# Kernel optimization log

Measured on AMD Instinct MI355X. Metric: run time of the kernel, lower is better.

The kernel has to match this reference:

```python
import jax, jax.numpy as jnp
import numpy as np

K = 3          # kernel_size (forced by hardcoded padding=1 in query unfold)
PAD = 1        # padding
C_IN = 64      # conv in_channels (x has C_IN + 5 channels)
C_OUT = 128    # out_channels
B, H, W = 16, 32, 32


def unfold(x, k, pad=0, mode='constant'):
    """torch.nn.functional.unfold equivalent. x: (B,C,H,W) -> (B, C*k*k, L).
    Ordering matches torch: channel slowest, then kernel row, then kernel col."""
    if pad:
        x = jnp.pad(x, ((0, 0), (0, 0), (pad, pad), (pad, pad)), mode=mode)
    b, c, h, w = x.shape
    oh, ow = h - k + 1, w - k + 1
    # (B, C, k*k, oh, ow) with patch index i*k+j
    patches = jnp.stack([x[:, :, i:i + oh, j:j + ow]
                         for i in range(k) for j in range(k)], axis=2)
    return patches.reshape(b, c * k * k, oh * ow)


def conv2d(x, w, b, pad):
    out = jax.lax.conv_general_dilated(
        x, w, window_strides=(1, 1), padding=[(pad, pad), (pad, pad)],
        dimension_numbers=('NCHW', 'OIHW', 'NCHW'))
    return out + b[None, :, None, None]


def setup_inputs() -> dict:
    key = jax.random.key(0)
    ks = jax.random.split(key, 6)
    fan1 = C_IN * K * K
    fan2 = C_OUT * 1 * 1
    return {
        'x': jax.random.normal(ks[0], (B, C_IN + 5, H, W), jnp.float32),
        'conv_w': jax.random.normal(ks[1], (C_OUT, C_IN, K, K), jnp.float32) / np.sqrt(fan1),
        'conv_b': jax.random.normal(ks[2], (C_OUT,), jnp.float32) * 0.01,
        'conv2_w': jax.random.normal(ks[3], (1, C_OUT, 1, 1), jnp.float32) / np.sqrt(fan2),
        'conv2_b': jax.random.normal(ks[4], (1,), jnp.float32) * 0.01,
        'shapes_kernel': jax.random.uniform(ks[5], (1, C_OUT, K * K * 5, 1), jnp.float32),
    }


def reference(x, conv_w, conv_b, conv2_w, conv2_b, shapes_kernel):
    k, pad = K, PAD
    center = k * k // 2

    conv_out = conv2d(x[:, :-5], conv_w, conv_b, pad)          # (B, C_OUT, H', W')
    b, cout, oh, ow = conv_out.shape
    L = oh * ow

    # shape-channel windows (replication-padded), center-relative positions
    sw = unfold(x[:, -5:], k, pad, 'edge').reshape(b, 5, k * k, L)
    sw = sw.at[:, 0:2].add(-sw[:, 0:2, center:center + 1])

    # L1 distance of each window to each learned shape kernel
    sd = jnp.abs(sw.reshape(b, 1, 5 * k * k, L) - shapes_kernel).sum(axis=2)  # (B, C_OUT, L)
    sd = sd.reshape(b, cout, oh, ow)

    saf = jax.nn.relu(conv_out / (sd + 1.0))                    # shape_attended_features

    q = conv2d(saf, conv2_w, conv2_b, 0) / jnp.sqrt(jnp.float32(cout))  # (B, 1, H', W')
    qu = jax.nn.softmax(unfold(q, k, 1), axis=1)[:, None]       # (B, 1, k*k, L), zero-padded

    u_mean = unfold(x[:, -5:-3], k, pad, 'edge').reshape(b, 2, k * k, L)
    means = (u_mean * qu).sum(axis=2)                           # (B, 2, L)

    v1 = (unfold(x[:, -3:-1], k, pad, 'edge').reshape(b, 2, k * k, L) * qu).sum(axis=2)
    v2 = (((u_mean - means[:, :, None, :]) ** 2) * qu).sum(axis=2)
    var = v1 + v2                                               # (B, 2, L)

    c1 = (unfold(x[:, -1:], k, pad, 'edge').reshape(b, 1, k * k, L) * qu).sum(axis=2)
    c2 = ((u_mean[:, 0:1] - means[:, 0:1, None, :]) *
          (u_mean[:, 1:2] - means[:, 1:2, None, :]) * qu).sum(axis=2)
    covar = c1 + c2                                             # (B, 1, L)

    agg = jnp.concatenate([means, var, covar], axis=1).reshape(b, 5, oh, ow)
    return jnp.concatenate([saf, agg], axis=1)                  # (B, C_OUT+5, H', W')
```

## Files before the change

kernel.cpp:

```cpp
#include <hip/hip_runtime.h>
#include <math.h>

#define CI 64
#define CO 128
#define CX 69
#define LPIX 1024

typedef __attribute__((ext_vector_type(8))) short bf16x8;
typedef __attribute__((ext_vector_type(4))) float f32x4;

#define WMF_OFF  0
#define SKT_OFF  147456
#define QP_OFF   (147456 + 23040)

__device__ __forceinline__ unsigned short f2bf(float f) {
  unsigned u = __float_as_uint(f);
  unsigned r = (u + 0x7fffu + ((u >> 16) & 1u)) >> 16;
  return (unsigned short)r;
}

__launch_bounds__(256)
__global__ void prepW(const float* __restrict__ cwg,
                      const float* __restrict__ skg,
                      unsigned short* __restrict__ wmf,
                      float* __restrict__ skt) {
  int i = blockIdx.x * 256 + threadIdx.x;
  if (i < 128 * 9 * 64) {
    int co = i / 576, rem = i - co * 576;
    int tap = rem >> 6, ci = rem & 63;
    wmf[i] = f2bf(cwg[co * 576 + ci * 9 + tap]);
  } else {
    int d = i - 128 * 9 * 64;
    if (d < 45 * 128) {
      int j = d >> 7, co = d & 127;
      skt[j * 128 + co] = skg[co * 45 + j];
    }
  }
}

__launch_bounds__(512, 4)
__global__ void convFused(const float* __restrict__ xg,
                          const unsigned short* __restrict__ wmfg,
                          const float* __restrict__ cbg,
                          const float* __restrict__ w2g,
                          const float* __restrict__ sktg,
                          float* __restrict__ qp,
                          float* __restrict__ outg) {
  __shared__ char arena[18432];
  __shared__ float lds_sx[5 * 144];
  __shared__ float qred[8][64];

  unsigned short* ldsB = (unsigned short*)arena;
  float* lds_c = (float*)arena;

  const int tid = threadIdx.x;
  const int blk = blockIdx.x;
  const int coh = blk & 1;
  const int rp  = (blk >> 1) & 15;
  const int b   = blk >> 5;
  const int r0  = rp * 2;

  const int w    = tid >> 6;
  const int lane = tid & 63;
  const int rsel = w >> 2;
  const int ct   = w & 3;
  const int n16  = lane & 15;
  const int kq   = lane >> 4;

  const float* xb = xg + (size_t)b * CX * LPIX;
  const float* xs = xb + CI * LPIX;

  bf16x8 areg[2][9];
  {
    const unsigned short* abase =
        wmfg + (size_t)(coh * 64 + ct * 16 + n16) * 576 + kq * 8;
    #pragma unroll
    for (int ch = 0; ch < 2; ++ch)
      #pragma unroll
      for (int tap = 0; tap < 9; ++tap)
        areg[ch][tap] = *(const bf16x8*)(abase + tap * 64 + ch * 32);
  }

  {
    const int row  = tid >> 7;
    const int cip  = (tid >> 2) & 31;
    const int colq = tid & 3;
    const int ci   = cip * 2;
    const int c0   = colq * 8;
    const int grow = r0 - 1 + row;
    f32x4 u0a = {}, u0b = {}, u1a = {}, u1b = {};
    if ((unsigned)grow < 32u) {
      const float* p0 = xb + ci * LPIX + grow * 32 + c0;
      u0a = *(const f32x4*)p0;          u0b = *(const f32x4*)(p0 + 4);
      u1a = *(const f32x4*)(p0 + LPIX); u1b = *(const f32x4*)(p0 + LPIX + 4);
    }
    #pragma unroll
    for (int cc = 0; cc < 8; ++cc) {
      float f0 = (cc < 4) ? u0a[cc] : u0b[cc - 4];
      float f1 = (cc < 4) ? u1a[cc] : u1b[cc - 4];
      unsigned v = (unsigned)f2bf(f0) | ((unsigned)f2bf(f1) << 16);
      const int slot  = c0 + cc + 1;
      const int gslot = ((ci >> 3) << 3) ^ ((slot & 7) << 3);
      ((unsigned*)ldsB)[(((row * 36 + slot) << 6) + gslot + (ci & 7)) >> 1] = v;
    }
    {
      const int prw = tid >> 7;
      const int s4  = (tid >> 5) & 3;
      const int sl  = (s4 == 0) ? 0 : (32 + s4);
      const int ci2 = (tid & 31) * 2;
      const int gsl = ((ci2 >> 3) << 3) ^ ((sl & 7) << 3);
      ((unsigned*)ldsB)[(((prw * 36 + sl) << 6) + gsl + (ci2 & 7)) >> 1] = 0;
    }
  }

  for (int idx = tid; idx < 5 * 144; idx += 512) {
    int c = idx / 144, rem = idx - c * 144;
    int s = rem / 36, j = rem - s * 36;
    int hh = r0 - 1 + s; hh = hh < 0 ? 0 : (hh > 31 ? 31 : hh);
    int col = j - 1;     col = col < 0 ? 0 : (col > 31 ? 31 : col);
    lds_sx[idx] = xs[c * LPIX + hh * 32 + col];
  }
  __syncthreads();

  f32x4 acc[2] = {};
  #pragma unroll
  for (int tap = 0; tap < 9; ++tap) {
    const int dr = tap / 3, dc = tap % 3;
    const int rowst = rsel + dr;
    #pragma unroll
    for (int ch = 0; ch < 2; ++ch) {
      const int g = (ch << 2) + kq;
      #pragma unroll
      for (int pt = 0; pt < 2; ++pt) {
        const int slot = pt * 16 + n16 + dc;
        const int gs = (g ^ (slot & 7)) << 3;
        bf16x8 bfr = *(const bf16x8*)(ldsB + ((rowst * 36 + slot) << 6) + gs);
        acc[pt] = __builtin_amdgcn_mfma_f32_16x16x32_bf16(areg[ch][tap], bfr,
                                                          acc[pt], 0, 0, 0);
      }
    }
  }
  __syncthreads();

  #pragma unroll
  for (int pt = 0; pt < 2; ++pt) {
    const int pxl = rsel * 32 + pt * 16 + n16;
    const int cog = ct * 4 + kq;
    const int sg  = cog ^ (pxl & 7);
    *(f32x4*)&lds_c[pxl * 64 + sg * 4] = acc[pt];
  }
  __syncthreads();

  const int wS   = __builtin_amdgcn_readfirstlane(w);
  const int co0g = coh * 64 + wS * 8;
  const int pxl  = lane;

  float cvals[8];
  #pragma unroll
  for (int g = 0; g < 2; ++g) {
    const int cog = wS * 2 + g;
    const int sg  = cog ^ (pxl & 7);
    *(f32x4*)&cvals[g * 4] = *(const f32x4*)&lds_c[pxl * 64 + sg * 4];
  }

  const int xbase = (pxl >> 5) * 36 + (pxl & 31);
  float swv[45];
  {
    const float c0 = lds_sx[0 * 144 + 37 + xbase];
    const float c1 = lds_sx[1 * 144 + 37 + xbase];
    #pragma unroll
    for (int c = 0; c < 5; ++c) {
      float ctr = (c == 0) ? c0 : ((c == 1) ? c1 : 0.f);
      #pragma unroll
      for (int s = 0; s < 3; ++s)
        #pragma unroll
        for (int dc = 0; dc < 3; ++dc)
          swv[c * 9 + s * 3 + dc] = lds_sx[c * 144 + s * 36 + dc + xbase] - ctr;
    }
  }

  float sd[8];
  #pragma unroll
  for (int k = 0; k < 8; ++k) sd[k] = 0.f;
  const float* skt = sktg + co0g;
  #pragma unroll
  for (int j = 0; j < 45; ++j) {
    const float sv = swv[j];
    #pragma unroll
    for (int k = 0; k < 8; ++k)
      sd[k] += fabsf(sv - skt[j * 128 + k]);
  }

  float qpv = 0.f;
  float* ob = outg + ((size_t)b * 133 + co0g) * LPIX + (r0 + (pxl >> 5)) * 32 + (pxl & 31);
  #pragma unroll
  for (int k = 0; k < 8; ++k) {
    float v = (cvals[k] + cbg[co0g + k]) * __builtin_amdgcn_rcpf(sd[k] + 1.0f);
    v = v > 0.f ? v : 0.f;
    ob[(size_t)k * LPIX] = v;
    qpv = fmaf(v, w2g[co0g + k], qpv);
  }

  qred[w][lane] = qpv;
  __syncthreads();
  if (tid < 64) {
    float q = 0.f;
    #pragma unroll
    for (int w8 = 0; w8 < 8; ++w8) q += qred[w8][tid];
    qp[coh * 16384 + b * LPIX + r0 * 32 + tid] = q;
  }
}

__launch_bounds__(64)
__global__ void statsB(const float* __restrict__ xg,
                       const float* __restrict__ qp,
                       const float* __restrict__ b2g,
                       float* __restrict__ outg) {
  const int gid = blockIdx.x * 64 + threadIdx.x;
  const int b = gid >> 10;
  const int h = (gid >> 5) & 31;
  const int w = gid & 31;

  const float b2 = b2g[0];
  const float* q0 = qp + (size_t)b * LPIX;
  float qv[9];
  float m = -1e30f;
  #pragma unroll
  for (int t = 0; t < 9; ++t) {
    int hh = h + t / 3 - 1, wc = w + t % 3 - 1;
    float v = 0.f;
    if ((unsigned)hh < 32u && (unsigned)wc < 32u) {
      int off = hh * 32 + wc;
      v = (q0[off] + q0[16384 + off] + b2) * 0.08838834764831845f;
    }
    qv[t] = v;
    m = fmaxf(m, v);
  }
  float ssum = 0.f;
  #pragma unroll
  for (int t = 0; t < 9; ++t) { qv[t] = expf(qv[t] - m); ssum += qv[t]; }
  const float inv = 1.f / ssum;

  const float* xs = xg + ((size_t)b * CX + CI) * LPIX;
  float um0[9], um1[9];
  float m0 = 0.f, m1 = 0.f, v1a = 0.f, v1b = 0.f, c1 = 0.f;
  #pragma unroll
  for (int t = 0; t < 9; ++t) {
    int hh = h + t / 3 - 1; hh = hh < 0 ? 0 : (hh > 31 ? 31 : hh);
    int wc = w + t % 3 - 1; wc = wc < 0 ? 0 : (wc > 31 ? 31 : wc);
    int off = hh * 32 + wc;
    float quv = qv[t] * inv;
    qv[t] = quv;
    float a0 = xs[off];
    float a1 = xs[LPIX + off];
    float b0 = xs[2 * LPIX + off];
    float b1 = xs[3 * LPIX + off];
    float cc = xs[4 * LPIX + off];
    um0[t] = a0; um1[t] = a1;
    m0 = fmaf(a0, quv, m0);
    m1 = fmaf(a1, quv, m1);
    v1a = fmaf(b0, quv, v1a);
    v1b = fmaf(b1, quv, v1b);
    c1 = fmaf(cc, quv, c1);
  }
  float var0 = v1a, var1 = v1b, cov = c1;
  #pragma unroll
  for (int t = 0; t < 9; ++t) {
    float d0 = um0[t] - m0, d1 = um1[t] - m1;
    var0 = fmaf(d0 * d0, qv[t], var0);
    var1 = fmaf(d1 * d1, qv[t], var1);
    cov  = fmaf(d0 * d1, qv[t], cov);
  }
  float* ob = outg + ((size_t)b * 133 + 128) * LPIX + h * 32 + w;
  ob[0 * LPIX] = m0;
  ob[1 * LPIX] = m1;
  ob[2 * LPIX] = var0;
  ob[3 * LPIX] = var1;
  ob[4 * LPIX] = cov;
}

extern "C" void kernel_launch(void* const* d_in, const int* in_sizes, int n_in,
                              void* d_out, int out_size, void* d_ws, size_t ws_size,
                              hipStream_t stream) {
  const float* x  = (const float*)d_in[0];
  const float* cw = (const float*)d_in[1];
  const float* cb = (const float*)d_in[2];
  const float* w2 = (const float*)d_in[3];
  const float* b2 = (const float*)d_in[4];
  const float* sk = (const float*)d_in[5];
  float* out = (float*)d_out;

  unsigned short* wmf = (unsigned short*)((char*)d_ws + WMF_OFF);
  float* skt = (float*)((char*)d_ws + SKT_OFF);
  float* qp  = (float*)((char*)d_ws + QP_OFF);

  prepW<<<dim3(311), dim3(256), 0, stream>>>(cw, sk, wmf, skt);
  convFused<<<dim3(512), dim3(512), 0, stream>>>(x, wmf, cb, w2, skt, qp, out);
  statsB<<<dim3(256), dim3(64), 0, stream>>>(x, qp, b2, out);
}
```

Measured before the change: 32.42 us.

## Fold weight prep kernel into conv kernel with in-register bf16 conversion

Removes the separate prepW launch that repacked conv weights to bf16 and transposed the shape kernels. The conv kernel now loads the original fp32 weights directly, gathers the per-tap elements and converts them with v_cvt_pk_bf16_f32 in registers, and it reads shape kernels in their original co-major layout. The launch bound is relaxed from 4 to 2 blocks per CU so the kernel has room for the extra registers used by the conversion buffer. This saves one kernel launch and a global round trip. In exchange, every block rereads twice as many weight bytes, occupancy may drop, and the shape-kernel reads are now strided across channels.

```diff
diff --git a/kernel.cpp b/kernel.cpp
--- a/kernel.cpp
+++ b/kernel.cpp
@@ -9,9 +9,7 @@
 typedef __attribute__((ext_vector_type(8))) short bf16x8;
 typedef __attribute__((ext_vector_type(4))) float f32x4;
 
-#define WMF_OFF  0
-#define SKT_OFF  147456
-#define QP_OFF   (147456 + 23040)
+#define QP_OFF   0
 
 __device__ __forceinline__ unsigned short f2bf(float f) {
   unsigned u = __float_as_uint(f);
@@ -19,31 +17,12 @@
   return (unsigned short)r;
 }
 
-__launch_bounds__(256)
-__global__ void prepW(const float* __restrict__ cwg,
-                      const float* __restrict__ skg,
-                      unsigned short* __restrict__ wmf,
-                      float* __restrict__ skt) {
-  int i = blockIdx.x * 256 + threadIdx.x;
-  if (i < 128 * 9 * 64) {
-    int co = i / 576, rem = i - co * 576;
-    int tap = rem >> 6, ci = rem & 63;
-    wmf[i] = f2bf(cwg[co * 576 + ci * 9 + tap]);
-  } else {
-    int d = i - 128 * 9 * 64;
-    if (d < 45 * 128) {
-      int j = d >> 7, co = d & 127;
-      skt[j * 128 + co] = skg[co * 45 + j];
-    }
-  }
-}
-
-__launch_bounds__(512, 4)
+__launch_bounds__(512, 2)
 __global__ void convFused(const float* __restrict__ xg,
-                          const unsigned short* __restrict__ wmfg,
+                          const float* __restrict__ cwg,
                           const float* __restrict__ cbg,
                           const float* __restrict__ w2g,
-                          const float* __restrict__ sktg,
+                          const float* __restrict__ skg,
                           float* __restrict__ qp,
                           float* __restrict__ outg) {
   __shared__ char arena[18432];
@@ -72,13 +51,29 @@
 
   bf16x8 areg[2][9];
   {
-    const unsigned short* abase =
-        wmfg + (size_t)(coh * 64 + ct * 16 + n16) * 576 + kq * 8;
-    #pragma unroll
-    for (int ch = 0; ch < 2; ++ch)
-      #pragma unroll
-      for (int tap = 0; tap < 9; ++tap)
-        areg[ch][tap] = *(const bf16x8*)(abase + tap * 64 + ch * 32);
+    const float* wbase = cwg + (size_t)(coh * 64 + ct * 16 + n16) * 576 + kq * 72;
+    #pragma unroll
+    for (int ch = 0; ch < 2; ++ch) {
+      f32x4 buf[18];
+      #pragma unroll
+      for (int i = 0; i < 18; ++i)
+        buf[i] = *(const f32x4*)(wbase + ch * 288 + i * 4);
+      #pragma unroll
+      for (int tap = 0; tap < 9; ++tap) {
+        union { unsigned u[4]; bf16x8 v; } cv;
+        #pragma unroll
+        for (int p = 0; p < 4; ++p) {
+          const int e0 = (2 * p) * 9 + tap;
+          const int e1 = (2 * p + 1) * 9 + tap;
+          float lo = buf[e0 >> 2][e0 & 3];
+          float hi = buf[e1 >> 2][e1 & 3];
+          unsigned r;
+          asm("v_cvt_pk_bf16_f32 %0, %1, %2" : "=v"(r) : "v"(lo), "v"(hi));
+          cv.u[p] = r;
+        }
+        areg[ch][tap] = cv.v;
+      }
+    }
   }
 
   {
@@ -181,14 +176,13 @@
 
   float sd[8];
   #pragma unroll
-  for (int k = 0; k < 8; ++k) sd[k] = 0.f;
-  const float* skt = sktg + co0g;
-  #pragma unroll
-  for (int j = 0; j < 45; ++j) {
-    const float sv = swv[j];
-    #pragma unroll
-    for (int k = 0; k < 8; ++k)
-      sd[k] += fabsf(sv - skt[j * 128 + k]);
+  for (int k = 0; k < 8; ++k) {
+    const float* kp = skg + (size_t)(co0g + k) * 45;
+    float s = 0.f;
+    #pragma unroll
+    for (int j = 0; j < 45; ++j)
+      s += fabsf(swv[j] - kp[j]);
+    sd[k] = s;
   }
 
   float qpv = 0.f;
@@ -290,11 +284,8 @@
   const float* sk = (const float*)d_in[5];
   float* out = (float*)d_out;
 
-  unsigned short* wmf = (unsigned short*)((char*)d_ws + WMF_OFF);
-  float* skt = (float*)((char*)d_ws + SKT_OFF);
-  float* qp  = (float*)((char*)d_ws + QP_OFF);
-
-  prepW<<<dim3(311), dim3(256), 0, stream>>>(cw, sk, wmf, skt);
-  convFused<<<dim3(512), dim3(512), 0, stream>>>(x, wmf, cb, w2, skt, qp, out);
+  float* qp = (float*)((char*)d_ws + QP_OFF);
+
+  convFused<<<dim3(512), dim3(512), 0, stream>>>(x, cw, cb, w2, sk, qp, out);
   statsB<<<dim3(256), dim3(64), 0, stream>>>(x, qp, b2, out);
 }
```

After: 36.43 us. 12.4% more time.
